# Optimization experiments

Hardware: AMD Instinct MI355X
Metric: run time of the kernel (lower is better)

Reference implementation:

```python
import jax, jax.numpy as jnp
import numpy as np

B, N, D, H = 4, 2048, 512, 8
KD = D // H  # per-head key/value dim = 64
NORM = 1.0 / np.sqrt(KD).astype(np.float32)


def setup_inputs() -> dict:
    key = jax.random.key(0)
    kq, km, k1, k2, k3 = jax.random.split(key, 5)
    s = 1.0 / np.sqrt(D)
    return {
        "queries": jax.random.normal(kq, (B, N, D), dtype=jnp.float32),
        "mask": jax.random.randint(km, (B, N, N), 0, 2).astype(jnp.bool_),
        "Wq": jax.random.normal(k1, (D, D), dtype=jnp.float32) * s,
        "Wk": jax.random.normal(k2, (D, D), dtype=jnp.float32) * s,
        "Wc": jax.random.normal(k3, (D, D), dtype=jnp.float32) * s,
    }


def reference(queries, mask, Wq, Wk, Wc):
    # Self-attention path (keys=None, values=None): V uses key_embed (Wk).
    Q = (queries @ Wq.T).reshape(B, N, H, KD)  # [B,N,H,kd]
    K = (queries @ Wk.T).reshape(B, N, H, KD)
    V = K  # original code: V = key_embed(queries) when values is None
    scores = NORM * jnp.einsum("bqhd,bkhd->bhqk", Q, K)  # [B,H,N,N]
    scores = jnp.where(mask[:, None, :, :], -jnp.inf, scores)
    attn = jax.nn.softmax(scores, axis=-1)
    out = jnp.einsum("bhqk,bkhd->bqhd", attn, V).reshape(B, N, H * KD)
    return out @ Wc.T  # [B,N,D]
```

## Files before the change

### kernel.cpp

```cpp
#include <hip/hip_runtime.h>
#include <hip/hip_bf16.h>
#include <math.h>

#define B_ 4
#define N_ 2048
#define D_ 512
#define H_ 8
#define NORM2_ 0.18033688011112042f

typedef __attribute__((ext_vector_type(8))) short short8;
typedef __attribute__((ext_vector_type(4))) float f32x4;
#define MFMA16(a, b, c) __builtin_amdgcn_mfma_f32_16x16x32_bf16(a, b, c, 0, 0, 0)
#define EXP2(x) __builtin_amdgcn_exp2f(x)

static __device__ __forceinline__ uint32_t pk2(float lo, float hi) {
  __hip_bfloat162 h = __float22bfloat162_rn(make_float2(lo, hi));
  return *(reinterpret_cast<uint32_t*>(&h));
}

static __device__ __forceinline__ void async16(const ushort* lds, const ushort* g) {
  __builtin_amdgcn_global_load_lds(
      (const __attribute__((address_space(1))) uint32_t*)g,
      (__attribute__((address_space(3))) uint32_t*)(ushort*)lds, 16, 0, 0);
}

__global__ __launch_bounds__(256) void prep(const float* __restrict__ q,
                                            const int* __restrict__ mask,
                                            const float* __restrict__ wq,
                                            const float* __restrict__ wk,
                                            const float* __restrict__ wc,
                                            ushort* __restrict__ Xb,
                                            ushort* __restrict__ Wb,
                                            uint32_t* __restrict__ pk) {
  const int bx = blockIdx.x;
  if (bx < 2048) {
    const int lane = threadIdx.x & 63;
    const int wid = ((bx << 8) + threadIdx.x) >> 6;
    for (int i = wid; i < 65536; i += 8192) {
      const int4 m = ((const int4*)mask)[(size_t)i * 64 + lane];
      uint32_t nib = (uint32_t)(m.x != 0) | ((uint32_t)(m.y != 0) << 1) |
                     ((uint32_t)(m.z != 0) << 2) | ((uint32_t)(m.w != 0) << 3);
      nib |= __shfl_xor(nib, 1) << 4;
      nib |= __shfl_xor(nib, 2) << 8;
      nib |= __shfl_xor(nib, 4) << 16;
      if ((lane & 7) == 0) pk[i * 8 + (lane >> 3)] = nib;
    }
  } else if (bx < 3072) {
    const int i = ((bx - 2048) << 8) + threadIdx.x;
    for (int j = i; j < 1048576; j += 262144) {
      const float4 v = ((const float4*)q)[j];
      uint2 o; o.x = pk2(v.x, v.y); o.y = pk2(v.z, v.w);
      ((uint2*)Xb)[j] = o;
    }
  } else {
    const int i = ((bx - 3072) << 8) + threadIdx.x;
    for (int j = i; j < 196608; j += 24576) {
      const int wi = j >> 16, off = j & 65535;
      const float* src = (wi == 0) ? wq : (wi == 1) ? wk : wc;
      const float4 v = ((const float4*)src)[off];
      uint2 o; o.x = pk2(v.x, v.y); o.y = pk2(v.z, v.w);
      ((uint2*)Wb)[j] = o;
    }
  }
}

__global__ __launch_bounds__(256) void merge(const ushort* __restrict__ P0,
                                             const float* __restrict__ l0,
                                             const float* __restrict__ l1,
                                             ushort* __restrict__ Ab) {
  const int j = (blockIdx.x << 8) + threadIdx.x;
  const int h = (j >> 3) & 7;
  const int tok = j >> 6;
  const int b = tok >> 11, n = tok & 2047;
  const int li = ((b * H_ + h) << 11) + n;
  const float inv = 1.f / (l0[li] + l1[li]);
  const uint4 a0 = ((const uint4*)P0)[j];
  const uint4 a1 = ((const uint4*)Ab)[j];
  uint4 o;
  const uint32_t* u0 = (const uint32_t*)&a0;
  const uint32_t* u1 = (const uint32_t*)&a1;
  uint32_t* uo = (uint32_t*)&o;
#pragma unroll
  for (int m = 0; m < 4; ++m) {
    const float lo = __uint_as_float(u0[m] << 16) + __uint_as_float(u1[m] << 16);
    const float hi = __uint_as_float(u0[m] & 0xFFFF0000u) +
                     __uint_as_float(u1[m] & 0xFFFF0000u);
    uo[m] = pk2(lo * inv, hi * inv);
  }
  ((uint4*)Ab)[j] = o;
}

template <int F32OUT>
__global__ __launch_bounds__(256) void gemm128(const ushort* __restrict__ X,
                                               const ushort* __restrict__ W0,
                                               const ushort* __restrict__ W1,
                                               void* __restrict__ C0,
                                               void* __restrict__ C1,
                                               float s0, float s1) {
  const ushort* Wp = (blockIdx.z == 0) ? W0 : W1;
  void* Cp = (blockIdx.z == 0) ? C0 : C1;
  const float sc = (blockIdx.z == 0) ? s0 : s1;
  const int t = threadIdx.x;
  const int w = t >> 6, lane = t & 63, quad = lane >> 4, c = lane & 15;
  const int wm = w & 1, wn = w >> 1;
  const int n0 = blockIdx.x * 128, m0 = blockIdx.y * 128;
  __shared__ __align__(16) ushort Xs[128][64];
  __shared__ __align__(16) ushort Ws[128][64];
  f32x4 acc[4][4];
#pragma unroll
  for (int i = 0; i < 4; ++i)
#pragma unroll
    for (int j = 0; j < 4; ++j) acc[i][j] = (f32x4){0.f, 0.f, 0.f, 0.f};

  for (int k0 = 0; k0 < D_; k0 += 64) {
    __syncthreads();
#pragma unroll
    for (int g = 0; g < 4; ++g) {
      const int id = w * 256 + g * 64 + lane;
      const int row = id >> 3, lch = id & 7;
      const int gch = lch ^ (row & 7);
      async16(&Xs[row][lch * 8], X + (size_t)(m0 + row) * D_ + k0 + gch * 8);
      async16(&Ws[row][lch * 8], Wp + (size_t)(n0 + row) * D_ + k0 + gch * 8);
    }
    __syncthreads();
#pragma unroll
    for (int s = 0; s < 2; ++s) {
      short8 af[4], bt[4];
#pragma unroll
      for (int i = 0; i < 4; ++i) {
        const int rA = wn * 64 + i * 16 + c;
        af[i] = *(const short8*)&Ws[rA][(((s * 4 + quad) ^ (rA & 7)) & 7) * 8];
        const int rB = wm * 64 + i * 16 + c;
        bt[i] = *(const short8*)&Xs[rB][(((s * 4 + quad) ^ (rB & 7)) & 7) * 8];
      }
#pragma unroll
      for (int i = 0; i < 4; ++i)
#pragma unroll
        for (int j = 0; j < 4; ++j) acc[i][j] = MFMA16(af[i], bt[j], acc[i][j]);
    }
  }
#pragma unroll
  for (int i = 0; i < 4; ++i)
#pragma unroll
    for (int j = 0; j < 4; ++j) {
      const size_t off =
          (size_t)(m0 + wm * 64 + j * 16 + c) * D_ + n0 + wn * 64 + i * 16 + quad * 4;
      if (F32OUT) {
        float4 v; v.x = acc[i][j][0]; v.y = acc[i][j][1]; v.z = acc[i][j][2]; v.w = acc[i][j][3];
        *(float4*)((float*)Cp + off) = v;
      } else {
        uint2 uv;
        uv.x = pk2(acc[i][j][0] * sc, acc[i][j][1] * sc);
        uv.y = pk2(acc[i][j][2] * sc, acc[i][j][3] * sc);
        *(uint2*)((ushort*)Cp + off) = uv;
      }
    }
}

__global__ __launch_bounds__(256) void attn_mfma(const ushort* __restrict__ Qb,
                                                 const ushort* __restrict__ Kb,
                                                 const uint32_t* __restrict__ pk,
                                                 ushort* __restrict__ P0,
                                                 ushort* __restrict__ P1,
                                                 float* __restrict__ l0,
                                                 float* __restrict__ l1) {
  const int qt64 = blockIdx.x >> 1, hf = blockIdx.x & 1;
  const int h = blockIdx.y, b = blockIdx.z;
  const int q0 = qt64 * 64;
  const int t = threadIdx.x;
  const int w = t >> 6, lane = t & 63, quad = lane >> 4, c = lane & 15;

  __shared__ __align__(16) ushort Ks[64][64];
  __shared__ __align__(16) uint32_t KtU[64][32];
  __shared__ __align__(16) ushort QP[4][16][72];
  ushort(*Qs)[64] = (ushort(*)[64]) & QP[0][0][0];
  ushort(*Pq)[16][72] = QP;

#pragma unroll
  for (int p = 0; p < 2; ++p) {
    const int id = t + p * 256;
    const int row = id >> 3, lch = id & 7, gch = lch ^ (row & 7);
    async16(&Qs[row][lch * 8], Qb + (size_t)(b * N_ + q0 + row) * D_ + h * 64 + gch * 8);
  }
  __syncthreads();
  const int rq = (w << 4) + c;
  const short8 bq0 = *(const short8*)&Qs[rq][((quad ^ (rq & 7)) & 7) * 8];
  const short8 bq1 = *(const short8*)&Qs[rq][(((4 + quad) ^ (rq & 7)) & 7) * 8];

  short8 vones;
#pragma unroll
  for (int i = 0; i < 8; ++i) vones[i] = (short)0x3F80;

  f32x4 o[4];
#pragma unroll
  for (int i = 0; i < 4; ++i) o[i] = (f32x4){0.f, 0.f, 0.f, 0.f};
  f32x4 o5 = (f32x4){0.f, 0.f, 0.f, 0.f};

  const int kp = t >> 3, ch = t & 7;
  const int r0 = 2 * kp, r1 = r0 + 1;
  const int ksw0 = ((ch ^ (r0 & 7)) & 7) * 8, ksw1 = ((ch ^ (r1 & 7)) & 7) * 8;
  const ushort* kb0 =
      Kb + (size_t)(b * N_ + hf * 1024 + 2 * kp) * D_ + h * 64 + ch * 8;
  const uint32_t* pkq =
      pk + ((size_t)(b * N_ + q0 + (w << 4) + c) << 6) + hf * 32;

  uint4 c0 = *(const uint4*)kb0;
  uint4 c1 = *(const uint4*)(kb0 + D_);
  uint2 cm = *(const uint2*)pkq;
  uint4 nx0, nx1; uint2 nxm;

  const int NT = 16;
  for (int kt = 0; kt < NT; ++kt) {
    __syncthreads();
    *(uint4*)&Ks[r0][ksw0] = c0;
    *(uint4*)&Ks[r1][ksw1] = c1;
    const uint32_t* a0 = (const uint32_t*)&c0;
    const uint32_t* a1 = (const uint32_t*)&c1;
#pragma unroll
    for (int m = 0; m < 4; ++m) {
      const uint32_t lo = __builtin_amdgcn_perm(a1[m], a0[m], 0x05040100);
      const uint32_t hi = __builtin_amdgcn_perm(a1[m], a0[m], 0x07060302);
      const int j0 = 2 * m, j1 = 2 * m + 1;
      KtU[ch * 8 + j0][(kp & 3) | ((((kp >> 2) ^ j0 ^ ch) & 7) << 2)] = lo;
      KtU[ch * 8 + j1][(kp & 3) | ((((kp >> 2) ^ j1 ^ ch) & 7) << 2)] = hi;
    }
    __syncthreads();

    if (kt + 1 < NT) {
      const ushort* kbn = kb0 + (size_t)(kt + 1) * 64 * D_;
      nx0 = *(const uint4*)kbn;
      nx1 = *(const uint4*)(kbn + D_);
      nxm = *(const uint2*)(pkq + (kt + 1) * 2);
    }

#pragma unroll
    for (int tI = 0; tI < 4; ++tI) {
      const int rk = tI * 16 + c;
      const short8 aK0 = *(const short8*)&Ks[rk][((quad ^ (rk & 7)) & 7) * 8];
      const short8 aK1 = *(const short8*)&Ks[rk][(((4 + quad) ^ (rk & 7)) & 7) * 8];
      f32x4 z = (f32x4){0.f, 0.f, 0.f, 0.f};
      z = MFMA16(aK0, bq0, z);
      z = MFMA16(aK1, bq1, z);
      const uint32_t mw = (tI < 2) ? cm.x : cm.y;
      const int bb = ((tI & 1) << 4) + quad * 4;
      uint32_t pb[4];
#pragma unroll
      for (int r = 0; r < 4; ++r) {
        const float e = EXP2(z[r]);
        pb[r] = ((mw >> (bb + r)) & 1u) ? 0u : __float_as_uint(e);
      }
      const uint32_t pw0 = __builtin_amdgcn_perm(pb[1], pb[0], 0x07060302);
      const uint32_t pw1 = __builtin_amdgcn_perm(pb[3], pb[2], 0x07060302);
      *(uint2*)&Pq[w][c][tI * 16 + quad * 4] = make_uint2(pw0, pw1);
    }

    const short8 bp0 = *(const short8*)&Pq[w][c][quad * 8];
    const short8 bp1 = *(const short8*)&Pq[w][c][32 + quad * 8];
    o5 = MFMA16(vones, bp0, o5);
    o5 = MFMA16(vones, bp1, o5);
#pragma unroll
    for (int dt = 0; dt < 4; ++dt) {
      const int dd = dt * 16 + c;
      const int g = (c & 7) ^ ((2 * dt + (c >> 3)) & 7);
      const short8 aV0 = *(const short8*)&KtU[dd][((quad ^ g) & 7) << 2];
      const short8 aV1 = *(const short8*)&KtU[dd][(((4 + quad) ^ g) & 7) << 2];
      o[dt] = MFMA16(aV0, bp0, o[dt]);
      o[dt] = MFMA16(aV1, bp1, o[dt]);
    }

    if (kt + 1 < NT) { c0 = nx0; c1 = nx1; cm = nxm; }
  }

  ushort* Pp = hf ? P1 : P0;
  float* lp = hf ? l1 : l0;
#pragma unroll
  for (int dt = 0; dt < 4; ++dt) {
    uint2 uv;
    uv.x = pk2(o[dt][0], o[dt][1]);
    uv.y = pk2(o[dt][2], o[dt][3]);
    *(uint2*)(Pp + (size_t)(b * N_ + q0 + (w << 4) + c) * D_ + h * 64 + dt * 16 + quad * 4) = uv;
  }
  if (quad == 0) lp[((b * H_ + h) << 11) + q0 + (w << 4) + c] = o5[0];
}

extern "C" void kernel_launch(void* const* d_in, const int* in_sizes, int n_in,
                              void* d_out, int out_size, void* d_ws, size_t ws_size,
                              hipStream_t stream) {
  const float* queries = (const float*)d_in[0];
  const int* mask = (const int*)d_in[1];
  const float* Wq = (const float*)d_in[2];
  const float* Wk = (const float*)d_in[3];
  const float* Wc = (const float*)d_in[4];
  float* out = (float*)d_out;

  const size_t nTok = (size_t)B_ * N_;
  const size_t nXD = nTok * D_;
  const size_t nW = (size_t)D_ * D_;
  ushort* Xb = (ushort*)d_ws;
  ushort* Wqb = Xb + nXD;
  ushort* Wkb = Wqb + nW;
  ushort* Wcb = Wkb + nW;
  ushort* Qb = Wcb + nW;
  ushort* Kb = Qb + nXD;
  ushort* Ab = Kb + nXD;
  uint32_t* pk = (uint32_t*)(Ab + nXD);
  ushort* P0 = Xb;
  ushort* P1 = Ab;
  float* l0 = (float*)Wqb;
  float* l1 = (float*)Wkb;

  prep<<<3168, 256, 0, stream>>>(queries, mask, Wq, Wk, Wc, Xb, Wqb, pk);
  gemm128<0><<<dim3(D_ / 128, (int)(nTok / 128), 2), 256, 0, stream>>>(
      Xb, Wqb, Wkb, Qb, Kb, NORM2_, 1.0f);
  attn_mfma<<<dim3(64, H_, B_), 256, 0, stream>>>(Qb, Kb, pk, P0, P1, l0, l1);
  merge<<<2048, 256, 0, stream>>>(P0, l0, l1, Ab);
  gemm128<1><<<dim3(D_ / 128, (int)(nTok / 128), 1), 256, 0, stream>>>(
      Ab, Wcb, nullptr, out, nullptr, 1.0f, 1.0f);
}
```

Before: 214.7 us.

## Double-buffer LDS tiles in projection GEMM to overlap loads with MFMA

Adds a second LDS buffer for the X and W tiles in gemm128 and issues the async global-to-LDS loads for the next K tile before computing on the current one. This drops one barrier per iteration and aims to hide global load latency behind the MFMA work. It doubles shared memory to 64KB per block, which may reduce occupancy. Correctness rests on the single barrier at the end of each iteration covering both load completion and buffer reuse.

```diff
diff --git a/kernel.cpp b/kernel.cpp
--- a/kernel.cpp
+++ b/kernel.cpp
@@ -104,41 +104,49 @@
   const int w = t >> 6, lane = t & 63, quad = lane >> 4, c = lane & 15;
   const int wm = w & 1, wn = w >> 1;
   const int n0 = blockIdx.x * 128, m0 = blockIdx.y * 128;
-  __shared__ __align__(16) ushort Xs[128][64];
-  __shared__ __align__(16) ushort Ws[128][64];
+  __shared__ __align__(16) ushort Xs[2][128][64];
+  __shared__ __align__(16) ushort Ws[2][128][64];
   f32x4 acc[4][4];
 #pragma unroll
   for (int i = 0; i < 4; ++i)
 #pragma unroll
     for (int j = 0; j < 4; ++j) acc[i][j] = (f32x4){0.f, 0.f, 0.f, 0.f};
 
-  for (int k0 = 0; k0 < D_; k0 += 64) {
-    __syncthreads();
-#pragma unroll
-    for (int g = 0; g < 4; ++g) {
-      const int id = w * 256 + g * 64 + lane;
-      const int row = id >> 3, lch = id & 7;
-      const int gch = lch ^ (row & 7);
-      async16(&Xs[row][lch * 8], X + (size_t)(m0 + row) * D_ + k0 + gch * 8);
-      async16(&Ws[row][lch * 8], Wp + (size_t)(n0 + row) * D_ + k0 + gch * 8);
-    }
-    __syncthreads();
+#define GSTAGE(bf, k0)                                                        \
+  do {                                                                        \
+    _Pragma("unroll") for (int g = 0; g < 4; ++g) {                           \
+      const int id = w * 256 + g * 64 + lane;                                 \
+      const int row = id >> 3, lch = id & 7;                                  \
+      const int gch = lch ^ (row & 7);                                        \
+      async16(&Xs[bf][row][lch * 8], X + (size_t)(m0 + row) * D_ + (k0) + gch * 8); \
+      async16(&Ws[bf][row][lch * 8], Wp + (size_t)(n0 + row) * D_ + (k0) + gch * 8); \
+    }                                                                         \
+  } while (0)
+
+  GSTAGE(0, 0);
+  __syncthreads();
+  const int NK = D_ / 64;
+  for (int kt = 0; kt < NK; ++kt) {
+    const int bf = kt & 1;
+    if (kt + 1 < NK) GSTAGE(bf ^ 1, (kt + 1) * 64);
 #pragma unroll
     for (int s = 0; s < 2; ++s) {
       short8 af[4], bt[4];
 #pragma unroll
       for (int i = 0; i < 4; ++i) {
         const int rA = wn * 64 + i * 16 + c;
-        af[i] = *(const short8*)&Ws[rA][(((s * 4 + quad) ^ (rA & 7)) & 7) * 8];
+        af[i] = *(const short8*)&Ws[bf][rA][(((s * 4 + quad) ^ (rA & 7)) & 7) * 8];
         const int rB = wm * 64 + i * 16 + c;
-        bt[i] = *(const short8*)&Xs[rB][(((s * 4 + quad) ^ (rB & 7)) & 7) * 8];
+        bt[i] = *(const short8*)&Xs[bf][rB][(((s * 4 + quad) ^ (rB & 7)) & 7) * 8];
       }
 #pragma unroll
       for (int i = 0; i < 4; ++i)
 #pragma unroll
         for (int j = 0; j < 4; ++j) acc[i][j] = MFMA16(af[i], bt[j], acc[i][j]);
     }
-  }
+    if (kt + 1 < NK) __syncthreads();
+  }
+#undef GSTAGE
 #pragma unroll
   for (int i = 0; i < 4; ++i)
 #pragma unroll
```

Result: faster. 209.6 us (-2.4%).
